# Kernel tuning notes

Hardware: AMD Instinct MI355X
Metric: run time of the kernel (lower is better)

## Reference

```python
import jax, jax.numpy as jnp
import numpy as np
from jax import lax

B, NPG, IN, OUT, ETYPES, STEPS, E = 16, 1024, 128, 256, 2, 6, 262144
N = B * NPG
CONCAT = IN + OUT
EPS = 1e-5


def setup_inputs() -> dict:
    key = jax.random.key(0)
    ks = jax.random.split(key, 24)
    s = 0.05
    return {
        "features": jax.random.normal(ks[0], (N, IN), jnp.float32),
        "src": jax.random.randint(ks[1], (E,), 0, N, jnp.int32),
        "dst": jax.random.randint(ks[2], (E,), 0, N, jnp.int32),
        "etype": jax.random.randint(ks[3], (E,), 0, ETYPES, jnp.int32),
        # GGNN per-etype linears (weight, bias) and GRUCell params
        "W_lin": jax.random.normal(ks[4], (ETYPES, OUT, OUT), jnp.float32) * s,
        "b_lin": jnp.zeros((ETYPES, OUT), jnp.float32),
        "W_ih": jax.random.normal(ks[5], (3 * OUT, OUT), jnp.float32) * s,
        "W_hh": jax.random.normal(ks[6], (3 * OUT, OUT), jnp.float32) * s,
        "b_ih": jnp.zeros((3 * OUT,), jnp.float32),
        "b_hh": jnp.zeros((3 * OUT,), jnp.float32),
        # conv branch on h_i (OUT channels)
        "conv1_w": jax.random.normal(ks[7], (OUT, OUT, 3), jnp.float32) * s,
        "conv1_b": jnp.zeros((OUT,), jnp.float32),
        "conv2_w": jax.random.normal(ks[8], (OUT, OUT, 1), jnp.float32) * s,
        "conv2_b": jnp.zeros((OUT,), jnp.float32),
        # conv branch on c_i (CONCAT channels)
        "convc1_w": jax.random.normal(ks[9], (CONCAT, CONCAT, 3), jnp.float32) * s,
        "convc1_b": jnp.zeros((CONCAT,), jnp.float32),
        "convc2_w": jax.random.normal(ks[10], (CONCAT, CONCAT, 1), jnp.float32) * s,
        "convc2_b": jnp.zeros((CONCAT,), jnp.float32),
        # shared batchnorms (training-mode batch stats, affine params)
        "bn_g": jnp.ones((OUT,), jnp.float32),
        "bn_b": jnp.zeros((OUT,), jnp.float32),
        "bnc_g": jnp.ones((CONCAT,), jnp.float32),
        "bnc_b": jnp.zeros((CONCAT,), jnp.float32),
        # gating MLPs
        "mlpy_w": jax.random.normal(ks[11], (2, OUT), jnp.float32) * s,
        "mlpy_b": jnp.zeros((2,), jnp.float32),
        "mlpz_w": jax.random.normal(ks[12], (2, CONCAT), jnp.float32) * s,
        "mlpz_b": jnp.zeros((2,), jnp.float32),
    }


def _bn_relu(x, g, b):  # x: [B, C, L], training-mode BN (biased var)
    mean = x.mean(axis=(0, 2), keepdims=True)
    var = ((x - mean) ** 2).mean(axis=(0, 2), keepdims=True)
    xn = (x - mean) * lax.rsqrt(var + EPS)
    return jax.nn.relu(xn * g[None, :, None] + b[None, :, None])


def _conv1d(x, w, b):  # x: [B, C, L], w: [O, I, K]
    y = lax.conv_general_dilated(x, w, (1,), 'VALID',
                                 dimension_numbers=('NCH', 'OIH', 'NCH'))
    return y + b[None, :, None]


def _maxpool(x, k, s):
    return lax.reduce_window(x, -jnp.inf, lax.max, (1, 1, k), (1, 1, s), 'VALID')


def _forward(features, src, dst, etype, W_lin, b_lin, W_ih, W_hh, b_ih, b_hh,
             conv1_w, conv1_b, conv2_w, conv2_b, convc1_w, convc1_b,
             convc2_w, convc2_b, bn_g, bn_b, bnc_g, bnc_b,
             mlpy_w, mlpy_b, mlpz_w, mlpz_b):
    # --- GatedGraphConv (DGL semantics): pad, n_steps of msg-pass + GRUCell ---
    h = jnp.pad(features, ((0, 0), (0, OUT - IN)))  # [N, OUT]
    for _ in range(STEPS):
        # per-etype linear applied to all nodes: [ETYPES, N, OUT]
        Wh = jnp.einsum('nd,ekd->enk', h, W_lin) + b_lin[:, None, :]
        msg = Wh[etype, src]                              # [E, OUT] gather
        agg = jax.ops.segment_sum(msg, dst, num_segments=N)  # scatter-add
        gi = agg @ W_ih.T + b_ih
        gh = h @ W_hh.T + b_hh
        ir, iz, ig = jnp.split(gi, 3, axis=-1)
        hr, hz, hg = jnp.split(gh, 3, axis=-1)
        r = jax.nn.sigmoid(ir + hr)
        z = jax.nn.sigmoid(iz + hz)
        n = jnp.tanh(ig + r * hg)
        h = (1.0 - z) * n + z * h

    h_i = h.reshape(B, NPG, OUT)
    x_i = features.reshape(B, NPG, IN)
    c_i = jnp.concatenate([h_i, x_i], axis=-1)  # [B, NPG, CONCAT]

    hT = jnp.swapaxes(h_i, 1, 2)  # [B, OUT, NPG]
    Y1 = _maxpool(_bn_relu(_conv1d(hT, conv1_w, conv1_b), bn_g, bn_b), 3, 2)
    Y2 = jnp.swapaxes(_maxpool(_bn_relu(_conv1d(Y1, conv2_w, conv2_b), bn_g, bn_b), 2, 2), 1, 2)

    cT = jnp.swapaxes(c_i, 1, 2)  # [B, CONCAT, NPG]
    Z1 = _maxpool(_bn_relu(_conv1d(cT, convc1_w, convc1_b), bnc_g, bnc_b), 3, 2)
    Z2 = jnp.swapaxes(_maxpool(_bn_relu(_conv1d(Z1, convc2_w, convc2_b), bnc_g, bnc_b), 2, 2), 1, 2)

    before_avg = (Y2 @ mlpy_w.T + mlpy_b) * (Z2 @ mlpz_w.T + mlpz_b)  # [B, L, 2]
    return jax.nn.sigmoid(before_avg.mean(axis=1))  # [B, 2]


def reference(features, src, dst, etype, W_lin, b_lin, W_ih, W_hh, b_ih, b_hh,
              conv1_w, conv1_b, conv2_w, conv2_b, convc1_w, convc1_b,
              convc2_w, convc2_b, bn_g, bn_b, bnc_g, bnc_b,
              mlpy_w, mlpy_b, mlpz_w, mlpz_b):
    return _forward(features, src, dst, etype, W_lin, b_lin, W_ih, W_hh, b_ih, b_hh,
                    conv1_w, conv1_b, conv2_w, conv2_b, convc1_w, convc1_b,
                    convc2_w, convc2_b, bn_g, bn_b, bnc_g, bnc_b,
                    mlpy_w, mlpy_b, mlpz_w, mlpz_b)
```

## Files before the change

### kernel.cpp

```cpp
#include <hip/hip_runtime.h>
#include <math.h>

constexpr int Bn     = 16;
constexpr int NPG    = 1024;
constexpr int Nn     = Bn * NPG;
constexpr int FIN    = 128;
constexpr int FOUT   = 256;
constexpr int CCAT   = 384;
constexpr int STEPS  = 6;
constexpr int NE     = 262144;

using short8 = __attribute__((ext_vector_type(8))) short;
using f32x4  = __attribute__((ext_vector_type(4))) float;

static __device__ __forceinline__ unsigned short f2bf(float x) {
    union { float f; unsigned u; } v; v.f = x;
    unsigned r = (v.u + 0x7FFFu + ((v.u >> 16) & 1u)) >> 16;
    return (unsigned short)r;
}
static __device__ __forceinline__ float bf2f(unsigned short b) {
    union { unsigned u; float f; } v; v.u = ((unsigned)b) << 16;
    return v.f;
}
static __device__ __forceinline__ float sigm(float x) { return 1.f / (1.f + expf(-x)); }

static __device__ __forceinline__ void gload16(const void* g, void* l) {
    __builtin_amdgcn_global_load_lds(
        (const __attribute__((address_space(1))) void*)g,
        (__attribute__((address_space(3))) void*)l, 16, 0, 0);
}


__global__ void cvt_bf(const float* __restrict__ s, unsigned short* __restrict__ d, int n) {
    int i = blockIdx.x * 256 + threadIdx.x;
    if (i < n) d[i] = f2bf(s[i]);
}

__global__ void cvt_wcat(const float* __restrict__ Wih, const float* __restrict__ Whh,
                         unsigned short* __restrict__ Wcat) {
    int o = blockIdx.x * 256 + threadIdx.x;
    int k = o >> 9, j = o & 511;
    float v = (j < 256) ? Whh[(size_t)k * 256 + j] : Wih[(size_t)k * 256 + (j - 256)];
    Wcat[o] = f2bf(v);
}

__global__ void add_bias(const float* __restrict__ a, const float* __restrict__ b,
                         float* __restrict__ o, int n) {
    int i = blockIdx.x * 256 + threadIdx.x;
    if (i < n) o[i] = a[i] + b[i];
}

__global__ void cvt_wconv(const float* __restrict__ W, unsigned short* __restrict__ Wt,
                          int C, int KW, int n) {
    int o = blockIdx.x * 256 + threadIdx.x;
    if (o >= n) return;
    int c = o / (KW * C), rem = o % (KW * C);
    int kb = rem / C, i = rem % C;
    Wt[o] = f2bf(W[(size_t)(c * C + i) * KW + kb]);
}

__global__ void pad_h(const float* __restrict__ f, float* __restrict__ h,
                      unsigned short* __restrict__ Acat) {
    int i = blockIdx.x * 256 + threadIdx.x;
    int k = i & 255, n = i >> 8;
    float v = (k < FIN) ? f[(size_t)n * FIN + k] : 0.f;
    h[i] = v; Acat[(size_t)n * 512 + k] = f2bf(v);
}

__global__ void build_cb(const unsigned short* __restrict__ Acat, const float* __restrict__ f,
                         unsigned short* __restrict__ cb) {
    int idx = blockIdx.x * 256 + threadIdx.x;
    int c = idx % CCAT, n = idx / CCAT;
    cb[idx] = (c < FOUT) ? Acat[(size_t)n * 512 + c] : f2bf(f[(size_t)n * FIN + (c - FOUT)]);
}


__global__ void edge_count(const int* __restrict__ dst, int* __restrict__ deg) {
    int e = blockIdx.x * 256 + threadIdx.x;
    atomicAdd(&deg[dst[e]], 1);
}

__global__ __launch_bounds__(1024) void scan_deg(const int* __restrict__ deg,
                                                 int* __restrict__ rowptr,
                                                 int* __restrict__ cursor) {
    __shared__ int ps[1024];
    const int t = threadIdx.x;
    int loc[16]; int s = 0;
    const int base = t * 16;
#pragma unroll
    for (int i = 0; i < 16; ++i) { loc[i] = deg[base + i]; s += loc[i]; }
    ps[t] = s;
    __syncthreads();
    for (int off = 1; off < 1024; off <<= 1) {
        int add = (t >= off) ? ps[t - off] : 0;
        __syncthreads();
        ps[t] += add;
        __syncthreads();
    }
    int run = ps[t] - s;
#pragma unroll
    for (int i = 0; i < 16; ++i) { rowptr[base + i] = run; cursor[base + i] = run; run += loc[i]; }
    if (t == 1023) rowptr[16384] = run;
}

__global__ void edge_fill(const int* __restrict__ src, const int* __restrict__ dst,
                          const int* __restrict__ et, int* __restrict__ cursor,
                          int* __restrict__ widx) {
    int e = blockIdx.x * 256 + threadIdx.x;
    int slot = atomicAdd(&cursor[dst[e]], 1);
    widx[slot] = src[e] * 2 + et[e];
}

static __device__ __forceinline__ void gemm128_body(
    const unsigned short* __restrict__ Ab, const unsigned short* __restrict__ W,
    const float* __restrict__ bias, float* __restrict__ Cf,
    unsigned short* __restrict__ Cb, int Ctap, int lda, int L, int Lv, int N, int K,
    int outBf, int l0, int col0, unsigned short* As, unsigned short* Bs) {
    const int t = threadIdx.x;
    const int w = t >> 6, l = t & 63;
    const int lr = l & 15, lhi = l >> 4;
    const int wr = w >> 1, wc = w & 1;
    const int srow8 = l >> 3;
    const int scole = ((l & 7) ^ srow8) * 8;
    const int lx7 = l & 7;

    f32x4 acc[4][4] = {};

    for (int k0 = 0; k0 < K; k0 += 64) {
        const int kb = k0 / Ctap;
        const int i0 = k0 - kb * Ctap;
        __syncthreads();
#pragma unroll
        for (int p = 0; p < 4; ++p) {
            const int r = w * 32 + p * 8;
            int srow = l0 + r + srow8 + kb;
            srow = srow < L ? srow : L - 1;
            gload16(Ab + (size_t)srow * lda + i0 + scole, &As[r * 64]);
            gload16(W + (size_t)(col0 + r + srow8) * K + k0 + scole, &Bs[r * 64]);
        }
        __syncthreads();
        const int abase = (wr * 64 + lr) * 64;
        const int bbase = (wc * 64 + lr) * 64;
#pragma unroll
        for (int kk = 0; kk < 2; ++kk) {
            const int soff = ((kk * 4 + lhi) ^ lx7) * 8;
            short8 af[4], bw[4];
#pragma unroll
            for (int fi = 0; fi < 4; ++fi)
                af[fi] = *(const short8*)&As[abase + fi * 1024 + soff];
#pragma unroll
            for (int fj = 0; fj < 4; ++fj)
                bw[fj] = *(const short8*)&Bs[bbase + fj * 1024 + soff];
#pragma unroll
            for (int fi = 0; fi < 4; ++fi)
#pragma unroll
                for (int fj = 0; fj < 4; ++fj)
                    acc[fi][fj] = __builtin_amdgcn_mfma_f32_16x16x32_bf16(
                        af[fi], bw[fj], acc[fi][fj], 0, 0, 0);
        }
    }
    const int rb = lhi * 4;
#pragma unroll
    for (int fi = 0; fi < 4; ++fi)
#pragma unroll
        for (int fj = 0; fj < 4; ++fj) {
            const int gcol = col0 + wc * 64 + fj * 16 + lr;
            const float bv = bias[gcol];
#pragma unroll
            for (int rr = 0; rr < 4; ++rr) {
                const int grow = l0 + wr * 64 + fi * 16 + rb + rr;
                if (grow < Lv) {
                    float v = acc[fi][fj][rr] + bv;
                    const size_t o = (size_t)grow * N + gcol;
                    if (outBf) Cb[o] = f2bf(v);
                    else       Cf[o] = v;
                }
            }
        }
}

__global__ __launch_bounds__(256) void gemm128(
    const unsigned short* __restrict__ A, const unsigned short* __restrict__ W,
    const float* __restrict__ bias, float* __restrict__ Cf,
    unsigned short* __restrict__ Cb, int Ctap, int lda, int L, int Lv, int N, int K,
    int outBf) {
    __shared__ unsigned short As[128 * 64];
    __shared__ unsigned short Bs[128 * 64];
    const size_t zo = (size_t)blockIdx.z;
    gemm128_body(A + zo * (size_t)L * lda, W, bias,
                 Cf ? Cf + zo * (size_t)Lv * N : nullptr,
                 Cb ? Cb + zo * (size_t)Lv * N : nullptr,
                 Ctap, lda, L, Lv, N, K, outBf,
                 blockIdx.y * 128, blockIdx.x * 128, As, Bs);
}

__global__ __launch_bounds__(256) void gemm128_swz(
    const unsigned short* __restrict__ A, const unsigned short* __restrict__ W,
    const float* __restrict__ bias, unsigned short* __restrict__ Cb,
    int lda, int N, int K) {
    __shared__ unsigned short As[128 * 64];
    __shared__ unsigned short Bs[128 * 64];
    const int gX = gridDim.x;
    const int hId = blockIdx.x + gX * blockIdx.y;
    const int xcd = hId & 7, tt = hId >> 3;
    const int bx = tt % gX, by = xcd + 8 * (tt / gX);
    gemm128_body(A, W, bias, nullptr, Cb, lda, lda, Nn, Nn, N, K, 1,
                 by * 128, bx * 128, As, Bs);
}

__global__ __launch_bounds__(256) void gemm_gru(
    const unsigned short* __restrict__ Acat, const unsigned short* __restrict__ Wcat,
    const unsigned short* __restrict__ Whg, const float* __restrict__ bias_s,
    const float* __restrict__ bias_g, float* __restrict__ h,
    unsigned short* __restrict__ Anext) {
    __shared__ unsigned short As[64 * 64];
    __shared__ unsigned short Bs[256 * 64];
    const int hId = blockIdx.x + 4 * blockIdx.y;
    const int xcd = hId & 7, tt = hId >> 3;
    const int bx = tt & 3, by = xcd + 8 * (tt >> 2);
    const int l0 = by * 64, c0 = bx * 64;

    const int t = threadIdx.x;
    const int w = t >> 6, l = t & 63;
    const int lr = l & 15, lhi = l >> 4;
    const int srow8 = l >> 3;
    const int scole = ((l & 7) ^ srow8) * 8;
    const int lx7 = l & 7;

    f32x4 acc[16] = {};

#pragma unroll
    for (int k0 = 0; k0 < 512; k0 += 64) {
        __syncthreads();
#pragma unroll
        for (int p = 0; p < 2; ++p) {
            const int r = w * 16 + p * 8;
            gload16(Acat + (size_t)(l0 + r + srow8) * 512 + k0 + scole, &As[r * 64]);
        }
#pragma unroll
        for (int p = 0; p < 8; ++p) {
            const int r = w * 64 + p * 8;
            if (r < 192) {
                const int g = r >> 6;
                const int cr = (r & 63) + srow8;
                gload16(Wcat + (size_t)(g * 256 + c0 + cr) * 512 + k0 + scole, &Bs[r * 64]);
            } else if (k0 < 256) {
                const int cr = (r - 192) + srow8;
                gload16(Whg + (size_t)(c0 + cr) * 256 + k0 + scole, &Bs[r * 64]);
            }
        }
        __syncthreads();
        const int abase = (w * 16 + lr) * 64;
#pragma unroll
        for (int kk = 0; kk < 2; ++kk) {
            const int soff = ((kk * 4 + lhi) ^ lx7) * 8;
            short8 a0 = *(const short8*)&As[abase + soff];
#pragma unroll
            for (int g = 0; g < 4; ++g) {
                if (!(g == 3 && k0 >= 256)) {
#pragma unroll
                    for (int fj = 0; fj < 4; ++fj) {
                        short8 bb = *(const short8*)&Bs[(g * 64 + fj * 16 + lr) * 64 + soff];
                        acc[g * 4 + fj] = __builtin_amdgcn_mfma_f32_16x16x32_bf16(
                            a0, bb, acc[g * 4 + fj], 0, 0, 0);
                    }
                }
            }
        }
    }
    const int rb = lhi * 4;
#pragma unroll
    for (int fj = 0; fj < 4; ++fj) {
        const int c = c0 + fj * 16 + lr;
        const float br = bias_s[c];
        const float bz = bias_s[256 + c];
        const float bg = bias_s[512 + c];
        const float bh = bias_g[c];
#pragma unroll
        for (int rr = 0; rr < 4; ++rr) {
            const int grow = l0 + w * 16 + rb + rr;
            float sr = acc[0 * 4 + fj][rr] + br;
            float sz = acc[1 * 4 + fj][rr] + bz;
            float sg = acc[2 * 4 + fj][rr] + bg;
            float hg = acc[3 * 4 + fj][rr] + bh;
            float r = sigm(sr), z = sigm(sz);
            float nn = tanhf(sg - (1.f - r) * hg);
            const size_t ho = (size_t)grow * 256 + c;
            float hv = (1.f - z) * nn + z * h[ho];
            h[ho] = hv;
            Anext[(size_t)grow * 512 + c] = f2bf(hv);
        }
    }
}

__global__ __launch_bounds__(64) void gather_agg(
    const unsigned short* __restrict__ Whb, const int* __restrict__ rowptr,
    const int* __restrict__ widx, unsigned short* __restrict__ Acat) {
    const int n = blockIdx.x, t = threadIdx.x;
    const int s0 = rowptr[n], s1 = rowptr[n + 1];
    float p0[4] = {}, p1[4] = {}, p2[4] = {}, p3[4] = {};
    int s = s0;
    for (; s + 4 <= s1; s += 4) {
        const int w0 = widx[s], w1 = widx[s + 1], w2 = widx[s + 2], w3 = widx[s + 3];
        const ushort4 v0 = *(const ushort4*)(Whb + (size_t)w0 * 256 + t * 4);
        const ushort4 v1 = *(const ushort4*)(Whb + (size_t)w1 * 256 + t * 4);
        const ushort4 v2 = *(const ushort4*)(Whb + (size_t)w2 * 256 + t * 4);
        const ushort4 v3 = *(const ushort4*)(Whb + (size_t)w3 * 256 + t * 4);
        p0[0] += bf2f(v0.x); p0[1] += bf2f(v0.y); p0[2] += bf2f(v0.z); p0[3] += bf2f(v0.w);
        p1[0] += bf2f(v1.x); p1[1] += bf2f(v1.y); p1[2] += bf2f(v1.z); p1[3] += bf2f(v1.w);
        p2[0] += bf2f(v2.x); p2[1] += bf2f(v2.y); p2[2] += bf2f(v2.z); p2[3] += bf2f(v2.w);
        p3[0] += bf2f(v3.x); p3[1] += bf2f(v3.y); p3[2] += bf2f(v3.z); p3[3] += bf2f(v3.w);
    }
    for (; s < s1; ++s) {
        const int wi = widx[s];
        const ushort4 v = *(const ushort4*)(Whb + (size_t)wi * 256 + t * 4);
        p0[0] += bf2f(v.x); p0[1] += bf2f(v.y); p0[2] += bf2f(v.z); p0[3] += bf2f(v.w);
    }
    ushort4 o;
    o.x = f2bf(p0[0] + p1[0] + p2[0] + p3[0]);
    o.y = f2bf(p0[1] + p1[1] + p2[1] + p3[1]);
    o.z = f2bf(p0[2] + p1[2] + p2[2] + p3[2]);
    o.w = f2bf(p0[3] + p1[3] + p2[3] + p3[3]);
    *(ushort4*)(Acat + (size_t)n * 512 + 256 + t * 4) = o;
}

constexpr int NCHUNK = 128;
__global__ __launch_bounds__(256) void bn_part_cl(
    const float* __restrict__ X, float* __restrict__ pS, float* __restrict__ pQ,
    int C, int totalRows, int rowsPerChunk) {
    const int t  = threadIdx.x;
    const int cq = t & 31, rl = t >> 5;
    const int c0 = blockIdx.x * 128 + cq * 4;
    const int r0 = blockIdx.y * rowsPerChunk;
    const int r1 = min(r0 + rowsPerChunk, totalRows);
    float s0 = 0, s1 = 0, s2 = 0, s3 = 0, q0 = 0, q1 = 0, q2 = 0, q3 = 0;
    for (int r = r0 + rl; r < r1; r += 8) {
        float4 v = *(const float4*)(X + (size_t)r * C + c0);
        s0 += v.x; s1 += v.y; s2 += v.z; s3 += v.w;
        q0 += v.x * v.x; q1 += v.y * v.y; q2 += v.z * v.z; q3 += v.w * v.w;
    }
    __shared__ float ls[8][128], lq[8][128];
    ls[rl][cq * 4 + 0] = s0; ls[rl][cq * 4 + 1] = s1;
    ls[rl][cq * 4 + 2] = s2; ls[rl][cq * 4 + 3] = s3;
    lq[rl][cq * 4 + 0] = q0; lq[rl][cq * 4 + 1] = q1;
    lq[rl][cq * 4 + 2] = q2; lq[rl][cq * 4 + 3] = q3;
    __syncthreads();
    if (rl == 0) {
#pragma unroll
        for (int i = 0; i < 4; ++i) {
            const int c = cq * 4 + i;
            float ss = 0, qq = 0;
#pragma unroll
            for (int j = 0; j < 8; ++j) { ss += ls[j][c]; qq += lq[j][c]; }
            pS[(size_t)blockIdx.y * C + c0 + i] = ss;
            pQ[(size_t)blockIdx.y * C + c0 + i] = qq;
        }
    }
}

__global__ __launch_bounds__(128) void bn_reduce_cl(
    const float* __restrict__ pS, const float* __restrict__ pQ,
    float* __restrict__ mean, float* __restrict__ var, int C, int totalRows) {
    const int c = blockIdx.x, t = threadIdx.x;
    __shared__ float rs[128], rq[128];
    rs[t] = pS[(size_t)t * C + c];
    rq[t] = pQ[(size_t)t * C + c];
    __syncthreads();
    for (int st = 64; st; st >>= 1) {
        if (t < st) { rs[t] += rs[t + st]; rq[t] += rq[t + st]; }
        __syncthreads();
    }
    if (t == 0) {
        float m = rs[0] / totalRows;
        mean[c] = m;
        var[c]  = rq[0] / totalRows - m * m;
    }
}

__global__ void bnp_cl(const float* __restrict__ X, const float* __restrict__ mean,
                       const float* __restrict__ var, const float* __restrict__ g,
                       const float* __restrict__ bta, float* __restrict__ Of,
                       unsigned short* __restrict__ Ob, int C, int Lin, int Lout,
                       int Kp, int outBf) {
    int idx = blockIdx.x * 256 + threadIdx.x;
    if (idx >= Bn * Lout * C) return;
    int c = idx % C, j = (idx / C) % Lout, b = idx / (C * Lout);
    float sc = g[c] * rsqrtf(var[c] + 1e-5f);
    float sh = bta[c] - mean[c] * sc;
    const float* xb = X + ((size_t)b * Lin + j * 2) * C + c;
    float m = 0.f;
    for (int k = 0; k < Kp; ++k) m = fmaxf(m, xb[(size_t)k * C] * sc + sh);
    if (outBf) Ob[idx] = f2bf(m);
    else       Of[idx] = m;
}

__global__ void final_dot(const float* __restrict__ Y2, const float* __restrict__ Z2,
                          const float* __restrict__ wy, const float* __restrict__ by,
                          const float* __restrict__ wz, const float* __restrict__ bz,
                          float* __restrict__ prod) {
    const int b = blockIdx.y, j = blockIdx.x, t = threadIdx.x;
    float p0 = 0, p1 = 0, q0 = 0, q1 = 0;
    const float* yrow = Y2 + (size_t)(b * 255 + j) * FOUT;
    const float* zrow = Z2 + (size_t)(b * 255 + j) * CCAT;
    for (int c = t; c < FOUT; c += 128) {
        float v = yrow[c];
        p0 += v * wy[c]; p1 += v * wy[FOUT + c];
    }
    for (int c = t; c < CCAT; c += 128) {
        float v = zrow[c];
        q0 += v * wz[c]; q1 += v * wz[CCAT + c];
    }
    __shared__ float r0[128], r1[128], r2[128], r3[128];
    r0[t] = p0; r1[t] = p1; r2[t] = q0; r3[t] = q1;
    __syncthreads();
    for (int s = 64; s; s >>= 1) {
        if (t < s) { r0[t] += r0[t + s]; r1[t] += r1[t + s]; r2[t] += r2[t + s]; r3[t] += r3[t + s]; }
        __syncthreads();
    }
    if (t == 0) {
        float y0 = r0[0] + by[0], y1 = r1[0] + by[1];
        float z0 = r2[0] + bz[0], z1 = r3[0] + bz[1];
        prod[((size_t)b * 255 + j) * 2 + 0] = y0 * z0;
        prod[((size_t)b * 255 + j) * 2 + 1] = y1 * z1;
    }
}

__global__ void final_out(const float* __restrict__ prod, float* __restrict__ out) {
    const int b = blockIdx.x, t = threadIdx.x;
    const int w = t >> 6, lane = t & 63;
    float s = 0.f;
    for (int j = lane; j < 255; j += 64) s += prod[((size_t)b * 255 + j) * 2 + w];
#pragma unroll
    for (int off = 32; off; off >>= 1) s += __shfl_down(s, off);
    if (lane == 0) out[b * 2 + w] = 1.f / (1.f + expf(-s / 255.f));
}

extern "C" void kernel_launch(void* const* d_in, const int* in_sizes, int n_in,
                              void* d_out, int out_size, void* d_ws, size_t ws_size,
                              hipStream_t stream) {
    (void)in_sizes; (void)n_in; (void)out_size; (void)ws_size;
    const float* features = (const float*)d_in[0];
    const int*   src      = (const int*)d_in[1];
    const int*   dst      = (const int*)d_in[2];
    const int*   etype    = (const int*)d_in[3];
    const float* W_lin    = (const float*)d_in[4];
    const float* b_lin    = (const float*)d_in[5];
    const float* W_ih     = (const float*)d_in[6];
    const float* W_hh     = (const float*)d_in[7];
    const float* b_ih     = (const float*)d_in[8];
    const float* b_hh     = (const float*)d_in[9];
    const float* conv1_w  = (const float*)d_in[10];
    const float* conv1_b  = (const float*)d_in[11];
    const float* conv2_w  = (const float*)d_in[12];
    const float* conv2_b  = (const float*)d_in[13];
    const float* convc1_w = (const float*)d_in[14];
    const float* convc1_b = (const float*)d_in[15];
    const float* convc2_w = (const float*)d_in[16];
    const float* convc2_b = (const float*)d_in[17];
    const float* bn_g     = (const float*)d_in[18];
    const float* bn_b     = (const float*)d_in[19];
    const float* bnc_g    = (const float*)d_in[20];
    const float* bnc_b    = (const float*)d_in[21];
    const float* mlpy_w   = (const float*)d_in[22];
    const float* mlpy_b   = (const float*)d_in[23];
    const float* mlpz_w   = (const float*)d_in[24];
    const float* mlpz_b   = (const float*)d_in[25];

    float* ws = (float*)d_ws;
    float*          h      = ws;
    unsigned short* Acat0  = (unsigned short*)(ws + 4194304);
    float*          bufA   = ws + 8388608;
    float*          bufB   = ws + 20971520;
    unsigned short* Wlin_b = (unsigned short*)(ws + 33554432);
    unsigned short* Whh_b  = (unsigned short*)(ws + 33554432) + 131072;
    unsigned short* Wcat_b = (unsigned short*)(ws + 33554432) + 327680;
    float*          bias_s = ws + 33950000;
    int*            ib     = (int*)(ws + 34000000);
    int* deg    = ib;
    int* cursor = ib + 16384;
    int* rowptr = ib + 32768;
    int* widx   = ib + 49160;
    float* sreg = ws + 34500000;
    float* meanb = sreg;
    float* varb  = sreg + 384;
    float* pS    = sreg + 1024;
    float* pQ    = sreg + 50176;
    float* prod  = sreg + 99328;

    unsigned short* Whb   = (unsigned short*)bufA;
    unsigned short* Acat1 = (unsigned short*)(bufA + 4194304);
    const unsigned short* Whg = Whh_b + 512 * 256;

    cvt_bf<<<512,  256, 0, stream>>>(W_lin, Wlin_b, 131072);
    cvt_bf<<<768,  256, 0, stream>>>(W_hh,  Whh_b,  196608);
    cvt_wcat<<<1536, 256, 0, stream>>>(W_ih, W_hh, Wcat_b);
    add_bias<<<3, 256, 0, stream>>>(b_ih, b_hh, bias_s, 768);
    pad_h<<<Nn * FOUT / 256, 256, 0, stream>>>(features, h, Acat0);

    hipMemsetAsync(deg, 0, 16384 * sizeof(int), stream);
    edge_count<<<NE / 256, 256, 0, stream>>>(dst, deg);
    scan_deg<<<1, 1024, 0, stream>>>(deg, rowptr, cursor);
    edge_fill<<<NE / 256, 256, 0, stream>>>(src, dst, etype, cursor, widx);

    unsigned short* Acur = Acat0;
    unsigned short* Anxt = Acat1;
    for (int s6 = 0; s6 < STEPS; ++s6) {
        gemm128_swz<<<dim3(4, 128), 256, 0, stream>>>(
            Acur, Wlin_b, b_lin, Whb, 512, 512, 256);
        gather_agg<<<Nn, 64, 0, stream>>>(Whb, rowptr, widx, Acur);
        gemm_gru<<<dim3(4, 256), 256, 0, stream>>>(
            Acur, Wcat_b, Whg, bias_s, b_hh + 512, h, Anxt);
        unsigned short* tmp = Acur; Acur = Anxt; Anxt = tmp;
    }

    unsigned short* cb    = (unsigned short*)ws;
    float*          Yc1   = bufA;
    unsigned short* P1y   = (unsigned short*)(bufA + 4186112);
    float*          Yc2   = bufA + 5230592;
    float*          Y2    = bufA + 7319552;
    float*          Z2    = bufA + 8364032;
    float*          Zc1   = bufB;
    unsigned short* P1z   = (unsigned short*)(bufB + 6279168);
    float*          Zc2   = bufB + 7845888;
    unsigned short* Wcv   = (unsigned short*)(bufB + 11000000);
    unsigned short* c1b   = Wcv;
    unsigned short* c2b   = Wcv + 196608;
    unsigned short* cc1b  = Wcv + 262144;
    unsigned short* cc2b  = Wcv + 704512;

    cvt_wconv<<<768,  256, 0, stream>>>(conv1_w,  c1b,  FOUT, 3, FOUT * FOUT * 3);
    cvt_wconv<<<256,  256, 0, stream>>>(conv2_w,  c2b,  FOUT, 1, FOUT * FOUT);
    cvt_wconv<<<1728, 256, 0, stream>>>(convc1_w, cc1b, CCAT, 3, CCAT * CCAT * 3);
    cvt_wconv<<<576,  256, 0, stream>>>(convc2_w, cc2b, CCAT, 1, CCAT * CCAT);
    build_cb<<<Nn * CCAT / 256, 256, 0, stream>>>(Acat0, features, cb);

    const int rows1 = Bn * 1022;
    const int rows2 = Bn * 510;
    const int rpc1  = (rows1 + NCHUNK - 1) / NCHUNK;
    const int rpc2  = (rows2 + NCHUNK - 1) / NCHUNK;

    gemm128<<<dim3(2, 8, Bn), 256, 0, stream>>>(Acat0, c1b, conv1_b, Yc1, nullptr,
                                                FOUT, 512, 1024, 1022, FOUT, 768, 0);
    bn_part_cl<<<dim3(FOUT / 128, NCHUNK), 256, 0, stream>>>(Yc1, pS, pQ, FOUT, rows1, rpc1);
    bn_reduce_cl<<<FOUT, 128, 0, stream>>>(pS, pQ, meanb, varb, FOUT, rows1);
    bnp_cl<<<(Bn * 510 * FOUT + 255) / 256, 256, 0, stream>>>(
        Yc1, meanb, varb, bn_g, bn_b, nullptr, P1y, FOUT, 1022, 510, 3, 1);
    gemm128<<<dim3(2, 4, Bn), 256, 0, stream>>>(P1y, c2b, conv2_b, Yc2, nullptr,
                                                FOUT, 256, 510, 510, FOUT, 256, 0);
    bn_part_cl<<<dim3(FOUT / 128, NCHUNK), 256, 0, stream>>>(Yc2, pS, pQ, FOUT, rows2, rpc2);
    bn_reduce_cl<<<FOUT, 128, 0, stream>>>(pS, pQ, meanb, varb, FOUT, rows2);
    bnp_cl<<<(Bn * 255 * FOUT + 255) / 256, 256, 0, stream>>>(
        Yc2, meanb, varb, bn_g, bn_b, Y2, nullptr, FOUT, 510, 255, 2, 0);

    gemm128<<<dim3(3, 8, Bn), 256, 0, stream>>>(cb, cc1b, convc1_b, Zc1, nullptr,
                                                CCAT, 384, 1024, 1022, CCAT, 1152, 0);
    bn_part_cl<<<dim3(CCAT / 128, NCHUNK), 256, 0, stream>>>(Zc1, pS, pQ, CCAT, rows1, rpc1);
    bn_reduce_cl<<<CCAT, 128, 0, stream>>>(pS, pQ, meanb, varb, CCAT, rows1);
    bnp_cl<<<(Bn * 510 * CCAT + 255) / 256, 256, 0, stream>>>(
        Zc1, meanb, varb, bnc_g, bnc_b, nullptr, P1z, CCAT, 1022, 510, 3, 1);
    gemm128<<<dim3(3, 4, Bn), 256, 0, stream>>>(P1z, cc2b, convc2_b, Zc2, nullptr,
                                                CCAT, 384, 510, 510, CCAT, 384, 0);
    bn_part_cl<<<dim3(CCAT / 128, NCHUNK), 256, 0, stream>>>(Zc2, pS, pQ, CCAT, rows2, rpc2);
    bn_reduce_cl<<<CCAT, 128, 0, stream>>>(pS, pQ, meanb, varb, CCAT, rows2);
    bnp_cl<<<(Bn * 255 * CCAT + 255) / 256, 256, 0, stream>>>(
        Zc2, meanb, varb, bnc_g, bnc_b, Z2, nullptr, CCAT, 510, 255, 2, 0);

    final_dot<<<dim3(255, Bn), 128, 0, stream>>>(Y2, Z2, mlpy_w, mlpy_b, mlpz_w, mlpz_b, prod);
    final_out<<<Bn, 128, 0, stream>>>(prod, (float*)d_out);
}
```

Measured before the change: 661.5 us.

## Merge Y and Z conv branches into paired kernel launches

The independent h-branch and c-branch conv/BN/pool pipelines are merged so that each stage (GEMM, BN partial sums, BN reduce, BN apply+pool) runs both branches in a single launch with a flattened block index. This halves the number of launches in the tail and fills the GPU better, since the small per-branch grids now run concurrently. Separate mean/var and partial-sum buffers are allocated per branch. The cost is branch divergence at block level and extra parameter passing.

```diff
diff --git a/kernel.cpp b/kernel.cpp
--- a/kernel.cpp
+++ b/kernel.cpp
@@ -179,21 +179,6 @@
         }
 }
 
-__global__ __launch_bounds__(256) void gemm128(
-    const unsigned short* __restrict__ A, const unsigned short* __restrict__ W,
-    const float* __restrict__ bias, float* __restrict__ Cf,
-    unsigned short* __restrict__ Cb, int Ctap, int lda, int L, int Lv, int N, int K,
-    int outBf) {
-    __shared__ unsigned short As[128 * 64];
-    __shared__ unsigned short Bs[128 * 64];
-    const size_t zo = (size_t)blockIdx.z;
-    gemm128_body(A + zo * (size_t)L * lda, W, bias,
-                 Cf ? Cf + zo * (size_t)Lv * N : nullptr,
-                 Cb ? Cb + zo * (size_t)Lv * N : nullptr,
-                 Ctap, lda, L, Lv, N, K, outBf,
-                 blockIdx.y * 128, blockIdx.x * 128, As, Bs);
-}
-
 __global__ __launch_bounds__(256) void gemm128_swz(
     const unsigned short* __restrict__ A, const unsigned short* __restrict__ W,
     const float* __restrict__ bias, unsigned short* __restrict__ Cb,
@@ -206,6 +191,31 @@
     const int bx = tt % gX, by = xcd + 8 * (tt / gX);
     gemm128_body(A, W, bias, nullptr, Cb, lda, lda, Nn, Nn, N, K, 1,
                  by * 128, bx * 128, As, Bs);
+}
+
+__global__ __launch_bounds__(256) void gemm128_pair2(
+    const unsigned short* __restrict__ A1, const unsigned short* __restrict__ W1,
+    const float* __restrict__ b1, float* __restrict__ C1,
+    int Ctap1, int lda1, int L1, int Lv1, int N1, int K1, int nx1, int ny1,
+    const unsigned short* __restrict__ A2, const unsigned short* __restrict__ W2,
+    const float* __restrict__ b2, float* __restrict__ C2,
+    int Ctap2, int lda2, int L2, int Lv2, int N2, int K2, int nx2, int ny2) {
+    __shared__ unsigned short As[128 * 64];
+    __shared__ unsigned short Bs[128 * 64];
+    int id = blockIdx.x;
+    const int n1 = nx1 * ny1 * Bn;
+    if (id < n1) {
+        int x = id % nx1, y = (id / nx1) % ny1, z = id / (nx1 * ny1);
+        gemm128_body(A1 + (size_t)z * L1 * lda1, W1, b1,
+                     C1 + (size_t)z * Lv1 * N1, nullptr,
+                     Ctap1, lda1, L1, Lv1, N1, K1, 0, y * 128, x * 128, As, Bs);
+    } else {
+        id -= n1;
+        int x = id % nx2, y = (id / nx2) % ny2, z = id / (nx2 * ny2);
+        gemm128_body(A2 + (size_t)z * L2 * lda2, W2, b2,
+                     C2 + (size_t)z * Lv2 * N2, nullptr,
+                     Ctap2, lda2, L2, Lv2, N2, K2, 0, y * 128, x * 128, As, Bs);
+    }
 }
 
 __global__ __launch_bounds__(256) void gemm_gru(
@@ -325,13 +335,14 @@
 }
 
 constexpr int NCHUNK = 128;
-__global__ __launch_bounds__(256) void bn_part_cl(
+
+static __device__ __forceinline__ void bn_part_body(
     const float* __restrict__ X, float* __restrict__ pS, float* __restrict__ pQ,
-    int C, int totalRows, int rowsPerChunk) {
+    int C, int totalRows, int rowsPerChunk, int bx, int by) {
     const int t  = threadIdx.x;
     const int cq = t & 31, rl = t >> 5;
-    const int c0 = blockIdx.x * 128 + cq * 4;
-    const int r0 = blockIdx.y * rowsPerChunk;
+    const int c0 = bx * 128 + cq * 4;
+    const int r0 = by * rowsPerChunk;
     const int r1 = min(r0 + rowsPerChunk, totalRows);
     float s0 = 0, s1 = 0, s2 = 0, s3 = 0, q0 = 0, q1 = 0, q2 = 0, q3 = 0;
     for (int r = r0 + rl; r < r1; r += 8) {
@@ -352,16 +363,36 @@
             float ss = 0, qq = 0;
 #pragma unroll
             for (int j = 0; j < 8; ++j) { ss += ls[j][c]; qq += lq[j][c]; }
-            pS[(size_t)blockIdx.y * C + c0 + i] = ss;
-            pQ[(size_t)blockIdx.y * C + c0 + i] = qq;
-        }
-    }
-}
-
-__global__ __launch_bounds__(128) void bn_reduce_cl(
-    const float* __restrict__ pS, const float* __restrict__ pQ,
-    float* __restrict__ mean, float* __restrict__ var, int C, int totalRows) {
-    const int c = blockIdx.x, t = threadIdx.x;
+            pS[(size_t)by * C + c0 + i] = ss;
+            pQ[(size_t)by * C + c0 + i] = qq;
+        }
+    }
+}
+
+__global__ __launch_bounds__(256) void bn_part_pair(
+    const float* __restrict__ X1, float* __restrict__ pS1, float* __restrict__ pQ1, int C1,
+    const float* __restrict__ X2, float* __restrict__ pS2, float* __restrict__ pQ2, int C2,
+    int totalRows, int rowsPerChunk) {
+    int id = blockIdx.x;
+    const int n1 = (C1 / 128) * NCHUNK;
+    if (id < n1)
+        bn_part_body(X1, pS1, pQ1, C1, totalRows, rowsPerChunk, id % (C1 / 128), id / (C1 / 128));
+    else {
+        id -= n1;
+        bn_part_body(X2, pS2, pQ2, C2, totalRows, rowsPerChunk, id % (C2 / 128), id / (C2 / 128));
+    }
+}
+
+__global__ __launch_bounds__(128) void bn_reduce_pair(
+    const float* __restrict__ pS1, const float* __restrict__ pQ1,
+    float* __restrict__ mean1, float* __restrict__ var1, int C1,
+    const float* __restrict__ pS2, const float* __restrict__ pQ2,
+    float* __restrict__ mean2, float* __restrict__ var2, int C2, int totalRows) {
+    int c = blockIdx.x;
+    const float* pS; const float* pQ; float* mean; float* var; int C;
+    if (c < C1) { pS = pS1; pQ = pQ1; mean = mean1; var = var1; C = C1; }
+    else { c -= C1; pS = pS2; pQ = pQ2; mean = mean2; var = var2; C = C2; }
+    const int t = threadIdx.x;
     __shared__ float rs[128], rq[128];
     rs[t] = pS[(size_t)t * C + c];
     rq[t] = pQ[(size_t)t * C + c];
@@ -377,12 +408,11 @@
     }
 }
 
-__global__ void bnp_cl(const float* __restrict__ X, const float* __restrict__ mean,
-                       const float* __restrict__ var, const float* __restrict__ g,
-                       const float* __restrict__ bta, float* __restrict__ Of,
-                       unsigned short* __restrict__ Ob, int C, int Lin, int Lout,
-                       int Kp, int outBf) {
-    int idx = blockIdx.x * 256 + threadIdx.x;
+static __device__ __forceinline__ void bnp_body(
+    const float* __restrict__ X, const float* __restrict__ mean,
+    const float* __restrict__ var, const float* __restrict__ g,
+    const float* __restrict__ bta, float* __restrict__ Of,
+    unsigned short* __restrict__ Ob, int C, int Lin, int Lout, int Kp, int outBf, int idx) {
     if (idx >= Bn * Lout * C) return;
     int c = idx % C, j = (idx / C) % Lout, b = idx / (C * Lout);
     float sc = g[c] * rsqrtf(var[c] + 1e-5f);
@@ -392,6 +422,26 @@
     for (int k = 0; k < Kp; ++k) m = fmaxf(m, xb[(size_t)k * C] * sc + sh);
     if (outBf) Ob[idx] = f2bf(m);
     else       Of[idx] = m;
+}
+
+__global__ void bnp_pair(
+    const float* __restrict__ X1, const float* __restrict__ mean1,
+    const float* __restrict__ var1, const float* __restrict__ g1,
+    const float* __restrict__ b1, float* __restrict__ Of1,
+    unsigned short* __restrict__ Ob1, int C1,
+    const float* __restrict__ X2, const float* __restrict__ mean2,
+    const float* __restrict__ var2, const float* __restrict__ g2,
+    const float* __restrict__ b2, float* __restrict__ Of2,
+    unsigned short* __restrict__ Ob2, int C2,
+    int Lin, int Lout, int Kp, int outBf) {
+    int id = blockIdx.x;
+    const int nb1 = (Bn * Lout * C1 + 255) / 256;
+    if (id < nb1)
+        bnp_body(X1, mean1, var1, g1, b1, Of1, Ob1, C1, Lin, Lout, Kp, outBf,
+                 id * 256 + threadIdx.x);
+    else
+        bnp_body(X2, mean2, var2, g2, b2, Of2, Ob2, C2, Lin, Lout, Kp, outBf,
+                 (id - nb1) * 256 + threadIdx.x);
 }
 
 __global__ void final_dot(const float* __restrict__ Y2, const float* __restrict__ Z2,
@@ -481,11 +531,15 @@
     int* rowptr = ib + 32768;
     int* widx   = ib + 49160;
     float* sreg = ws + 34500000;
-    float* meanb = sreg;
-    float* varb  = sreg + 384;
-    float* pS    = sreg + 1024;
-    float* pQ    = sreg + 50176;
-    float* prod  = sreg + 99328;
+    float* meanY = sreg;
+    float* varY  = sreg + 256;
+    float* meanZ = sreg + 512;
+    float* varZ  = sreg + 896;
+    float* pSy   = sreg + 1280;
+    float* pQy   = sreg + 34048;
+    float* pSz   = sreg + 66816;
+    float* pQz   = sreg + 115968;
+    float* prod  = sreg + 165120;
 
     unsigned short* Whb   = (unsigned short*)bufA;
     unsigned short* Acat1 = (unsigned short*)(bufA + 4194304);
@@ -539,31 +593,35 @@
     const int rpc1  = (rows1 + NCHUNK - 1) / NCHUNK;
     const int rpc2  = (rows2 + NCHUNK - 1) / NCHUNK;
 
-    gemm128<<<dim3(2, 8, Bn), 256, 0, stream>>>(Acat0, c1b, conv1_b, Yc1, nullptr,
-                                                FOUT, 512, 1024, 1022, FOUT, 768, 0);
-    bn_part_cl<<<dim3(FOUT / 128, NCHUNK), 256, 0, stream>>>(Yc1, pS, pQ, FOUT, rows1, rpc1);
-    bn_reduce_cl<<<FOUT, 128, 0, stream>>>(pS, pQ, meanb, varb, FOUT, rows1);
-    bnp_cl<<<(Bn * 510 * FOUT + 255) / 256, 256, 0, stream>>>(
-        Yc1, meanb, varb, bn_g, bn_b, nullptr, P1y, FOUT, 1022, 510, 3, 1);
-    gemm128<<<dim3(2, 4, Bn), 256, 0, stream>>>(P1y, c2b, conv2_b, Yc2, nullptr,
-                                                FOUT, 256, 510, 510, FOUT, 256, 0);
-    bn_part_cl<<<dim3(FOUT / 128, NCHUNK), 256, 0, stream>>>(Yc2, pS, pQ, FOUT, rows2, rpc2);
-    bn_reduce_cl<<<FOUT, 128, 0, stream>>>(pS, pQ, meanb, varb, FOUT, rows2);
-    bnp_cl<<<(Bn * 255 * FOUT + 255) / 256, 256, 0, stream>>>(
-        Yc2, meanb, varb, bn_g, bn_b, Y2, nullptr, FOUT, 510, 255, 2, 0);
-
-    gemm128<<<dim3(3, 8, Bn), 256, 0, stream>>>(cb, cc1b, convc1_b, Zc1, nullptr,
-                                                CCAT, 384, 1024, 1022, CCAT, 1152, 0);
-    bn_part_cl<<<dim3(CCAT / 128, NCHUNK), 256, 0, stream>>>(Zc1, pS, pQ, CCAT, rows1, rpc1);
-    bn_reduce_cl<<<CCAT, 128, 0, stream>>>(pS, pQ, meanb, varb, CCAT, rows1);
-    bnp_cl<<<(Bn * 510 * CCAT + 255) / 256, 256, 0, stream>>>(
-        Zc1, meanb, varb, bnc_g, bnc_b, nullptr, P1z, CCAT, 1022, 510, 3, 1);
-    gemm128<<<dim3(3, 4, Bn), 256, 0, stream>>>(P1z, cc2b, convc2_b, Zc2, nullptr,
-                                                CCAT, 384, 510, 510, CCAT, 384, 0);
-    bn_part_cl<<<dim3(CCAT / 128, NCHUNK), 256, 0, stream>>>(Zc2, pS, pQ, CCAT, rows2, rpc2);
-    bn_reduce_cl<<<CCAT, 128, 0, stream>>>(pS, pQ, meanb, varb, CCAT, rows2);
-    bnp_cl<<<(Bn * 255 * CCAT + 255) / 256, 256, 0, stream>>>(
-        Zc2, meanb, varb, bnc_g, bnc_b, Z2, nullptr, CCAT, 510, 255, 2, 0);
+    gemm128_pair2<<<2 * 8 * Bn + 3 * 8 * Bn, 256, 0, stream>>>(
+        Acat0, c1b, conv1_b, Yc1, FOUT, 512, 1024, 1022, FOUT, 768, 2, 8,
+        cb, cc1b, convc1_b, Zc1, CCAT, 384, 1024, 1022, CCAT, 1152, 3, 8);
+    bn_part_pair<<<(2 + 3) * NCHUNK, 256, 0, stream>>>(
+        Yc1, pSy, pQy, FOUT, Zc1, pSz, pQz, CCAT, rows1, rpc1);
+    bn_reduce_pair<<<FOUT + CCAT, 128, 0, stream>>>(
+        pSy, pQy, meanY, varY, FOUT, pSz, pQz, meanZ, varZ, CCAT, rows1);
+    {
+        const int nb1 = (Bn * 510 * FOUT + 255) / 256;
+        const int nb2 = (Bn * 510 * CCAT + 255) / 256;
+        bnp_pair<<<nb1 + nb2, 256, 0, stream>>>(
+            Yc1, meanY, varY, bn_g, bn_b, nullptr, P1y, FOUT,
+            Zc1, meanZ, varZ, bnc_g, bnc_b, nullptr, P1z, CCAT, 1022, 510, 3, 1);
+    }
+
+    gemm128_pair2<<<2 * 4 * Bn + 3 * 4 * Bn, 256, 0, stream>>>(
+        P1y, c2b, conv2_b, Yc2, FOUT, 256, 510, 510, FOUT, 256, 2, 4,
+        P1z, cc2b, convc2_b, Zc2, CCAT, 384, 510, 510, CCAT, 384, 3, 4);
+    bn_part_pair<<<(2 + 3) * NCHUNK, 256, 0, stream>>>(
+        Yc2, pSy, pQy, FOUT, Zc2, pSz, pQz, CCAT, rows2, rpc2);
+    bn_reduce_pair<<<FOUT + CCAT, 128, 0, stream>>>(
+        pSy, pQy, meanY, varY, FOUT, pSz, pQz, meanZ, varZ, CCAT, rows2);
+    {
+        const int nb1 = (Bn * 255 * FOUT + 255) / 256;
+        const int nb2 = (Bn * 255 * CCAT + 255) / 256;
+        bnp_pair<<<nb1 + nb2, 256, 0, stream>>>(
+            Yc2, meanY, varY, bn_g, bn_b, Y2, nullptr, FOUT,
+            Zc2, meanZ, varZ, bnc_g, bnc_b, Z2, nullptr, CCAT, 510, 255, 2, 0);
+    }
 
     final_dot<<<dim3(255, Bn), 128, 0, stream>>>(Y2, Z2, mlpy_w, mlpy_b, mlpz_w, mlpz_b, prod);
     final_out<<<Bn, 128, 0, stream>>>(prod, (float*)d_out);
```

Measured after the change: 609.0 us. -7.9%, faster.
